# Kernel optimization log

Hardware: AMD Instinct MI355X
Metric: run time of the kernel (lower is better)

## Reference

```python
import jax, jax.numpy as jnp
import numpy as np

D_MODEL = 1024
N_HEADS = 16
D_HEAD = D_MODEL // N_HEADS
B, T = 4, 2048


def layernorm(x, g, b, eps=1e-5):
    mu = jnp.mean(x, axis=-1, keepdims=True)
    var = jnp.mean((x - mu) ** 2, axis=-1, keepdims=True)
    return (x - mu) * jax.lax.rsqrt(var + eps) * g + b


def setup_inputs() -> dict:
    key = jax.random.key(0)
    ks = jax.random.split(key, 12)
    s_in = 1.0 / np.sqrt(D_MODEL)
    s_ff = 1.0 / np.sqrt(4 * D_MODEL)
    return {
        "x": jax.random.normal(ks[0], (B, T, D_MODEL), jnp.float32),
        "Wq": jax.random.normal(ks[1], (N_HEADS, D_MODEL, D_HEAD), jnp.float32) * s_in,
        "Wk": jax.random.normal(ks[2], (N_HEADS, D_MODEL, D_HEAD), jnp.float32) * s_in,
        "Wv": jax.random.normal(ks[3], (N_HEADS, D_MODEL, D_HEAD), jnp.float32) * s_in,
        "Wproj": jax.random.normal(ks[4], (D_MODEL, D_MODEL), jnp.float32) * s_in,
        "bproj": jnp.zeros((D_MODEL,), jnp.float32),
        "W1": jax.random.normal(ks[5], (D_MODEL, 4 * D_MODEL), jnp.float32) * s_in,
        "b1": jnp.zeros((4 * D_MODEL,), jnp.float32),
        "W2": jax.random.normal(ks[6], (4 * D_MODEL, D_MODEL), jnp.float32) * s_ff,
        "b2": jnp.zeros((D_MODEL,), jnp.float32),
        "g1": jnp.ones((D_MODEL,), jnp.float32),
        "beta1": jnp.zeros((D_MODEL,), jnp.float32),
        "g2": jnp.ones((D_MODEL,), jnp.float32),
        "beta2": jnp.zeros((D_MODEL,), jnp.float32),
    }


def reference(x, Wq, Wk, Wv, Wproj, bproj, W1, b1, W2, b2, g1, beta1, g2, beta2):
    Bb, Tt, C = x.shape
    # x = ln1(x); residual uses the NORMALIZED x (quirk of original module)
    x1 = layernorm(x, g1, beta1)
    # all heads at once: [B,H,T,Dh]
    q = jnp.einsum("btd,hdk->bhtk", x1, Wq)
    k = jnp.einsum("btd,hdk->bhtk", x1, Wk)
    v = jnp.einsum("btd,hdk->bhtk", x1, Wv)
    # NOTE: original scales by 1/sqrt(C) with C = d_model, not d_head
    wei = jnp.einsum("bhtk,bhsk->bhts", q, k) / np.sqrt(C).astype(np.float32)
    causal = jnp.tril(jnp.ones((Tt, Tt), bool))
    wei = jnp.where(causal, wei, -jnp.inf)
    wei = jax.nn.softmax(wei, axis=-1)
    attn = jnp.einsum("bhts,bhsk->bhtk", wei, v)  # [B,H,T,Dh]
    attn = attn.transpose(0, 2, 1, 3).reshape(Bb, Tt, C)  # concat heads
    sa = attn @ Wproj + bproj
    x2 = x1 + sa
    # x = ln2(x); residual again uses the normalized tensor
    x3 = layernorm(x2, g2, beta2)
    h = jax.nn.relu(x3 @ W1 + b1)
    ff = h @ W2 + b2
    return x3 + ff
```

## Files before the change

kernel.cpp:

```cpp
#include <hip/hip_runtime.h>
#include <cstdint>

typedef _Float16 f16;
typedef __attribute__((ext_vector_type(8))) _Float16 f16x8;
typedef __attribute__((ext_vector_type(4))) _Float16 f16x4;
typedef __attribute__((ext_vector_type(2))) _Float16 f16x2;
typedef __attribute__((ext_vector_type(4))) float f32x4;
typedef __attribute__((ext_vector_type(16))) float f32x16;

#define D_MODEL 1024
#define T_SEQ   2048
#define NTOK    8192
#define DFF     4096
#define DHEAD   64

struct alignas(16) H8 { f16 h[8]; };

__device__ __forceinline__ void load_lds16(const void* gp, void* lp) {
  __builtin_amdgcn_global_load_lds(
      (const __attribute__((address_space(1))) unsigned int*)(unsigned long long)(uintptr_t)gp,
      (__attribute__((address_space(3))) unsigned int*)(unsigned int)(uintptr_t)lp,
      16, 0, 0);
}

__device__ __forceinline__ void phase_bar() {
  asm volatile("" ::: "memory");
  __builtin_amdgcn_sched_barrier(0);
  __builtin_amdgcn_s_barrier();
  __builtin_amdgcn_sched_barrier(0);
  asm volatile("" ::: "memory");
}

__device__ __forceinline__ void wait_vm2() {
  asm volatile("s_waitcnt vmcnt(2)" ::: "memory");
  __builtin_amdgcn_sched_barrier(0);
}
__device__ __forceinline__ void wait_vm0() {
  asm volatile("s_waitcnt vmcnt(0)" ::: "memory");
  __builtin_amdgcn_sched_barrier(0);
}

__global__ __launch_bounds__(256) void transpose_all(
    const float* __restrict__ Wq, const float* __restrict__ Wk,
    const float* __restrict__ Wv, const float* __restrict__ Wproj,
    const float* __restrict__ W1, const float* __restrict__ W2,
    f16* __restrict__ Wqkv_t, f16* __restrict__ Wproj_t,
    f16* __restrict__ W1_t, f16* __restrict__ W2_t)
{
  __shared__ float tile[32][33];
  int b = blockIdx.x;
  const float* in; f16* out; int rows, cols, r0, c0;
  if (b < 3072) {
    int j = b >> 10;
    int local = b & 1023;
    int slice = local >> 6;
    int tl = local & 63;
    in  = (j == 0 ? Wq : (j == 1 ? Wk : Wv)) + (size_t)slice * 65536;
    out = Wqkv_t + (size_t)j * 1024 * 1024 + (size_t)slice * 65536;
    rows = 1024; cols = 64;
    r0 = (tl & 31) * 32; c0 = (tl >> 5) * 32;
  } else if (b < 4096) {
    int tl = b - 3072;
    in = Wproj; out = Wproj_t; rows = 1024; cols = 1024;
    r0 = (tl & 31) * 32; c0 = (tl >> 5) * 32;
  } else if (b < 8192) {
    int tl = b - 4096;
    in = W1; out = W1_t; rows = 1024; cols = 4096;
    r0 = (tl & 31) * 32; c0 = (tl >> 5) * 32;
  } else {
    int tl = b - 8192;
    in = W2; out = W2_t; rows = 4096; cols = 1024;
    r0 = (tl & 127) * 32; c0 = (tl >> 7) * 32;
  }
  int tx = threadIdx.x & 31, ty = threadIdx.x >> 5;
  #pragma unroll
  for (int i = 0; i < 4; ++i)
    tile[ty + i*8][tx] = in[(size_t)(r0 + ty + i*8)*cols + c0 + tx];
  __syncthreads();
  #pragma unroll
  for (int i = 0; i < 4; ++i)
    out[(size_t)(c0 + ty + i*8)*rows + r0 + tx] = (f16)tile[tx][ty + i*8];
}

__global__ __launch_bounds__(256) void ln_kernel(
    const float* __restrict__ x, const float* __restrict__ g, const float* __restrict__ b,
    float* __restrict__ outf, f16* __restrict__ outh)
{
  int row = blockIdx.x;
  const float* xr = x + (size_t)row * D_MODEL;
  int tid = threadIdx.x;
  float v[4];
  float s = 0.f;
  #pragma unroll
  for (int i = 0; i < 4; ++i) { v[i] = xr[tid + i*256]; s += v[i]; }
  #pragma unroll
  for (int off = 32; off > 0; off >>= 1) s += __shfl_down(s, off, 64);
  __shared__ float red1[4], red2[4];
  if ((tid & 63) == 0) red1[tid >> 6] = s;
  __syncthreads();
  float mean = (red1[0] + red1[1] + red1[2] + red1[3]) * (1.f / D_MODEL);
  float s2 = 0.f;
  #pragma unroll
  for (int i = 0; i < 4; ++i) { float d = v[i] - mean; s2 += d * d; }
  #pragma unroll
  for (int off = 32; off > 0; off >>= 1) s2 += __shfl_down(s2, off, 64);
  if ((tid & 63) == 0) red2[tid >> 6] = s2;
  __syncthreads();
  float var = (red2[0] + red2[1] + red2[2] + red2[3]) * (1.f / D_MODEL);
  float rstd = rsqrtf(var + 1e-5f);
  #pragma unroll
  for (int i = 0; i < 4; ++i) {
    int c = tid + i*256;
    float y = (v[i] - mean) * rstd * g[c] + b[c];
    outf[(size_t)row*D_MODEL + c] = y;
    outh[(size_t)row*D_MODEL + c] = (f16)y;
  }
}


#define STAGE_H(gbase, h, ldst, k0)                                            \
  { _Pragma("unroll")                                                          \
    for (int j_ = 0; j_ < 2; ++j_) {                                           \
      int c_  = tid + j_*512;                                                  \
      int rr_ = c_ >> 3;                                                       \
      int cg_ = (c_ & 7) ^ (rr_ & 7);                                          \
      load_lds16((gbase) + (size_t)((h)*128 + rr_) * K + (k0) + cg_*8,         \
                 (ldst) + (h)*128*64 + (size_t)(c_ & ~63) * 8);                \
    } }

#define LDS_A(bsel, mp)                                                        \
  { _Pragma("unroll")                                                          \
    for (int i_ = 0; i_ < 2; ++i_)                                             \
      _Pragma("unroll")                                                        \
      for (int ks_ = 0; ks_ < 4; ++ks_)                                        \
        fa[i_][ks_] = *(const f16x8*)(&As[bsel][                               \
            (wm + ((mp)*2 + i_)*32 + rl)*64 + (((ks_*2 + hl) ^ sw)*8)]); }

#define LDS_B(bsel, ni, fb)                                                    \
  { _Pragma("unroll")                                                          \
    for (int ks_ = 0; ks_ < 4; ++ks_)                                          \
      fb[ks_] = *(const f16x8*)(&Bs[bsel][                                     \
          (wn + (ni)*32 + rl)*64 + (((ks_*2 + hl) ^ sw)*8)]); }

#define MFMA8(mp, ni, fb)                                                      \
  { __builtin_amdgcn_s_setprio(1);                                             \
    _Pragma("unroll")                                                          \
    for (int ks_ = 0; ks_ < 4; ++ks_) {                                        \
      acc[(mp)*2+0][ni] = __builtin_amdgcn_mfma_f32_32x32x16_f16(              \
          fa[0][ks_], fb[ks_], acc[(mp)*2+0][ni], 0, 0, 0);                    \
      acc[(mp)*2+1][ni] = __builtin_amdgcn_mfma_f32_32x32x16_f16(              \
          fa[1][ks_], fb[ks_], acc[(mp)*2+1][ni], 0, 0, 0);                    \
    }                                                                          \
    __builtin_amdgcn_s_setprio(0); }

template<int MODE, int BN>
__global__ __launch_bounds__(512, 2) void gemm8(
    const f16* __restrict__ A, const f16* __restrict__ BT, int K,
    const float* __restrict__ bias, const float* __restrict__ resid,
    float* __restrict__ outf, f16* __restrict__ o0, f16* __restrict__ o1, f16* __restrict__ o2)
{
  constexpr int BM  = 256;
  constexpr int NWN = BN / 64;
  constexpr int MI  = (BM / (8 / NWN)) / 32;

  __shared__ __align__(16) f16 As[2][BM * 64];
  __shared__ __align__(16) f16 Bs[2][BN * 64];

  int tid  = threadIdx.x;
  int lane = tid & 63;
  int wave = tid >> 6;
  int rl = lane & 31, hl = lane >> 5;
  int sw = rl & 7;
  int wmi = wave / NWN, wni = wave % NWN;
  int wm = wmi * (MI * 32), wn = wni * 64;

  int gx  = gridDim.x;
  int gy  = gridDim.y;
  int nwg = gx * gy;
  int lin = blockIdx.x + gx * blockIdx.y;
  int sid = (nwg & 7) == 0 ? ((lin & 7) * (nwg >> 3) + (lin >> 3)) : lin;
  int bx  = sid / gy, by = sid % gy;

  size_t row0 = (size_t)bx * BM, col0 = (size_t)by * BN;
  const f16* a_base = A  + row0 * K;
  const f16* b_base = BT + col0 * K;
  int NT = K >> 6;

  f32x16 acc[MI][2];
  #pragma unroll
  for (int i = 0; i < MI; ++i)
    #pragma unroll
    for (int j = 0; j < 2; ++j)
      acc[i][j] = (f32x16)(0.f);

  f16x8 fa[2][4], fb0[4], fb1[4];

  if constexpr (BN == 256) {
    STAGE_H(a_base, 0, &As[0][0], 0);
    STAGE_H(a_base, 1, &As[0][0], 0);
    STAGE_H(b_base, 0, &Bs[0][0], 0);
    STAGE_H(b_base, 1, &Bs[0][0], 0);
    if (NT > 1) { STAGE_H(a_base, 0, &As[1][0], 64); wait_vm2(); }
    else        { wait_vm0(); }
    phase_bar();

    for (int t = 0; t < NT; ++t) {
      int cur = t & 1, nxt = cur ^ 1;
      int k1 = (t + 1) << 6, k2 = (t + 2) << 6;
      bool s1 = (t + 1) < NT, s2 = (t + 2) < NT;
      LDS_A(cur, 0); LDS_B(cur, 0, fb0);
      if (s1) STAGE_H(a_base, 1, &As[nxt][0], k1);
      phase_bar();
      MFMA8(0, 0, fb0);
      phase_bar();
      LDS_B(cur, 1, fb1);
      if (s1) STAGE_H(b_base, 0, &Bs[nxt][0], k1);
      phase_bar();
      MFMA8(0, 1, fb1);
      phase_bar();
      LDS_A(cur, 1);
      if (s1) STAGE_H(b_base, 1, &Bs[nxt][0], k1);
      phase_bar();
      MFMA8(1, 0, fb0);
      phase_bar();
      if (s2) STAGE_H(a_base, 0, &As[cur][0], k2);
      phase_bar();
      MFMA8(1, 1, fb1);
      if (s2) wait_vm2(); else wait_vm0();
      phase_bar();
    }
  } else {
    STAGE_H(a_base, 0, &As[0][0], 0);
    STAGE_H(a_base, 1, &As[0][0], 0);
    STAGE_H(b_base, 0, &Bs[0][0], 0);
    if (NT > 1) { STAGE_H(a_base, 0, &As[1][0], 64); wait_vm2(); }
    else        { wait_vm0(); }
    phase_bar();

    for (int t = 0; t < NT; t += 2) {
      int k1 = (t + 1) << 6, k2 = (t + 2) << 6, k3 = (t + 3) << 6;
      bool s1 = (t + 1) < NT, s2 = (t + 2) < NT, s3 = (t + 3) < NT;
      LDS_A(0, 0); LDS_B(0, 0, fb0);
      if (s1) { STAGE_H(a_base, 1, &As[1][0], k1); STAGE_H(b_base, 0, &Bs[1][0], k1); }
      phase_bar();
      MFMA8(0, 0, fb0);
      phase_bar();
      LDS_B(0, 1, fb1);
      if (s2) STAGE_H(a_base, 0, &As[0][0], k2);
      phase_bar();
      MFMA8(0, 1, fb1);
      if (s2) wait_vm2(); else wait_vm0();
      phase_bar();
      if (!s1) break;
      LDS_A(1, 0); LDS_B(1, 0, fb0);
      if (s2) { STAGE_H(a_base, 1, &As[0][0], k2); STAGE_H(b_base, 0, &Bs[0][0], k2); }
      phase_bar();
      MFMA8(0, 0, fb0);
      phase_bar();
      LDS_B(1, 1, fb1);
      if (s3) STAGE_H(a_base, 0, &As[1][0], k3);
      phase_bar();
      MFMA8(0, 1, fb1);
      if (s3) wait_vm2(); else wait_vm0();
      phase_bar();
    }
  }

  int rb = hl * 4;
  #pragma unroll
  for (int mi = 0; mi < MI; ++mi) {
    #pragma unroll
    for (int ni = 0; ni < 2; ++ni) {
      #pragma unroll
      for (int r = 0; r < 16; ++r) {
        size_t grow = row0 + wm + mi*32 + rb + (r & 3) + 8 * (r >> 2);
        size_t gcol = col0 + wn + ni*32 + rl;
        float v = acc[mi][ni][r];
        if constexpr (MODE == 0) {
          int sel = (int)(gcol >> 10);
          int hh  = ((int)gcol >> 6) & 15;
          int dd  = (int)gcol & 63;
          f16* dst = (sel == 0) ? o0 : ((sel == 1) ? o1 : o2);
          if (sel == 0) v *= 0.045084229f;
          size_t bh = (grow >> 11) * 16 + hh;
          dst[(bh * T_SEQ + (grow & 2047)) * DHEAD + dd] = (f16)v;
        } else if constexpr (MODE == 1 || MODE == 3) {
          size_t idx = grow * D_MODEL + gcol;
          outf[idx] = v + bias[gcol] + resid[idx];
        } else {
          float t = v + bias[gcol];
          o0[grow * (size_t)DFF + gcol] = (f16)(t > 0.f ? t : 0.f);
        }
      }
    }
  }
}

__global__ __launch_bounds__(256) void attn_mfma(
    const f16* __restrict__ qb, const f16* __restrict__ kb,
    const f16* __restrict__ vb, f16* __restrict__ attnb)
{
  constexpr int KT  = 64;
  constexpr int LDK = 72;
  __shared__ __align__(16) f16 Kl[2][KT * LDK];
  __shared__ __align__(16) f16 Vt[2][(DHEAD+16) * LDK];
  __shared__ __align__(16) f16 Pt[4 * 32 * LDK];

  int tid  = threadIdx.x;
  int lane = tid & 63, wave = tid >> 6;
  int n    = lane & 15, quad = lane >> 4;
  int quad4 = quad * 4;
  int bh   = blockIdx.x;
  int bxq  = blockIdx.y;

  const f16* qg = qb + (size_t)bh * T_SEQ * DHEAD;
  const f16* kg = kb + (size_t)bh * T_SEQ * DHEAD;
  const f16* vg = vb + (size_t)bh * T_SEQ * DHEAD;
  f16* Ptw = Pt + wave * 32 * LDK;
  size_t orow = (size_t)(bh >> 4) * T_SEQ;
  int hcol = (bh & 15) * DHEAD;

  int skey0 = tid >> 3,  sdq = tid & 7;
  int kp = tid & 31, dblk = tid >> 5;

  {
    int row = 64 + (tid >> 4);
    int colg = (tid & 15) * 4;
    f16 oneval = (f16)((tid >> 4) == 0 ? 1.0f : 0.0f);
    f16x4 fill = {oneval, oneval, oneval, oneval};
    *(f16x4*)(&Vt[0][0] + row * LDK + colg) = fill;
    *(f16x4*)(&Vt[1][0] + row * LDK + colg) = fill;
  }

  #pragma unroll
  for (int pass = 0; pass < 2; ++pass) {
    int qi = pass == 0 ? (15 - bxq) : bxq;
    int qw = qi * 128 + wave * 32;

    f16x8 qfrag[2][2];
    #pragma unroll
    for (int ni = 0; ni < 2; ++ni)
      #pragma unroll
      for (int kj = 0; kj < 2; ++kj)
        qfrag[ni][kj] = *(const f16x8*)(qg + (size_t)(qw + ni*16 + n)*DHEAD + kj*32 + quad*8);

    f32x4 o[2][4];
    f32x4 o4[2];
    #pragma unroll
    for (int mb = 0; mb < 2; ++mb) {
      #pragma unroll
      for (int di = 0; di < 4; ++di) o[mb][di] = f32x4{0.f,0.f,0.f,0.f};
      o4[mb] = f32x4{0.f,0.f,0.f,0.f};
    }

    int ntiles = 2 * qi + 2;

    uint4 kpre0 = *(const uint4*)(kg + (size_t)skey0 * DHEAD + sdq * 8);
    uint4 kpre1 = *(const uint4*)(kg + (size_t)(skey0 + 32) * DHEAD + sdq * 8);
    H8 vpa = *(const H8*)(vg + (size_t)(2*kp) * DHEAD + dblk * 8);
    H8 vpb = *(const H8*)(vg + (size_t)(2*kp) * DHEAD + DHEAD + dblk * 8);
    *(uint4*)(&Kl[0][0] + skey0 * LDK + sdq * 8) = kpre0;
    *(uint4*)(&Kl[0][0] + (skey0 + 32) * LDK + sdq * 8) = kpre1;
    #pragma unroll
    for (int e = 0; e < 8; ++e) {
      f16x2 pk2; pk2[0] = vpa.h[e]; pk2[1] = vpb.h[e];
      *(f16x2*)(&Vt[0][0] + (dblk*8 + e) * LDK + 2*kp) = pk2;
    }
    if (ntiles > 1) {
      kpre0 = *(const uint4*)(kg + (size_t)(KT + skey0) * DHEAD + sdq * 8);
      kpre1 = *(const uint4*)(kg + (size_t)(KT + skey0 + 32) * DHEAD + sdq * 8);
      vpa = *(const H8*)(vg + (size_t)(KT + 2*kp) * DHEAD + dblk * 8);
      vpb = *(const H8*)(vg + (size_t)(KT + 2*kp) * DHEAD + DHEAD + dblk * 8);
    }
    __syncthreads();

    for (int kt = 0; kt < ntiles; ++kt) {
      int kt0 = kt * KT;
      if (kt + 1 < ntiles) {
        f16* Kn = &Kl[(kt + 1) & 1][0];
        f16* Vn = &Vt[(kt + 1) & 1][0];
        *(uint4*)(Kn + skey0 * LDK + sdq * 8) = kpre0;
        *(uint4*)(Kn + (skey0 + 32) * LDK + sdq * 8) = kpre1;
        #pragma unroll
        for (int e = 0; e < 8; ++e) {
          f16x2 pk2; pk2[0] = vpa.h[e]; pk2[1] = vpb.h[e];
          *(f16x2*)(Vn + (dblk*8 + e) * LDK + 2*kp) = pk2;
        }
        if (kt + 2 < ntiles) {
          int nt0 = kt0 + 2 * KT;
          kpre0 = *(const uint4*)(kg + (size_t)(nt0 + skey0) * DHEAD + sdq * 8);
          kpre1 = *(const uint4*)(kg + (size_t)(nt0 + skey0 + 32) * DHEAD + sdq * 8);
          vpa = *(const H8*)(vg + (size_t)(nt0 + 2*kp) * DHEAD + dblk * 8);
          vpb = *(const H8*)(vg + (size_t)(nt0 + 2*kp) * DHEAD + DHEAD + dblk * 8);
        }
      }

      if (kt0 <= qw + 31) {
        const f16* Kc = &Kl[kt & 1][0];
        const f16* Vc = &Vt[kt & 1][0];
        bool need_mask = (kt0 + KT - 1) > qw;

        f32x4 st[4][2];
        #pragma unroll
        for (int mi = 0; mi < 4; ++mi)
          #pragma unroll
          for (int ni = 0; ni < 2; ++ni) st[mi][ni] = f32x4{0.f,0.f,0.f,0.f};
        __builtin_amdgcn_s_setprio(1);
        #pragma unroll
        for (int kj = 0; kj < 2; ++kj) {
          #pragma unroll
          for (int mi = 0; mi < 4; ++mi) {
            f16x8 kf = *(const f16x8*)(Kc + (mi*16 + n) * LDK + kj*32 + quad*8);
            #pragma unroll
            for (int ni = 0; ni < 2; ++ni)
              st[mi][ni] = __builtin_amdgcn_mfma_f32_16x16x32_f16(kf, qfrag[ni][kj], st[mi][ni], 0, 0, 0);
          }
        }
        __builtin_amdgcn_s_setprio(0);

        #pragma unroll
        for (int ni = 0; ni < 2; ++ni) {
          #pragma unroll
          for (int mi = 0; mi < 4; ++mi) {
            float pv[4];
            #pragma unroll
            for (int r = 0; r < 4; ++r) {
              float sv = st[mi][ni][r];
              if (need_mask) {
                int key = kt0 + mi*16 + quad4 + r;
                int qq  = qw  + ni*16 + n;
                if (key > qq) sv = -1e30f;
              }
              pv[r] = __builtin_amdgcn_exp2f(sv);
            }
            f16x2 lo = __builtin_bit_cast(f16x2, __builtin_amdgcn_cvt_pkrtz(pv[0], pv[1]));
            f16x2 hi = __builtin_bit_cast(f16x2, __builtin_amdgcn_cvt_pkrtz(pv[2], pv[3]));
            f16x4 pk; pk[0] = lo[0]; pk[1] = lo[1]; pk[2] = hi[0]; pk[3] = hi[1];
            *(f16x4*)(Ptw + (ni*16 + n) * LDK + mi*16 + quad4) = pk;
          }
        }

        __builtin_amdgcn_s_setprio(1);
        #pragma unroll
        for (int kj = 0; kj < 2; ++kj) {
          f16x8 pf[2];
          #pragma unroll
          for (int mb = 0; mb < 2; ++mb)
            pf[mb] = *(const f16x8*)(Ptw + (mb*16 + n) * LDK + kj*32 + quad*8);
          #pragma unroll
          for (int di = 0; di < 4; ++di) {
            f16x8 vf = *(const f16x8*)(Vc + (di*16 + n) * LDK + kj*32 + quad*8);
            #pragma unroll
            for (int mb = 0; mb < 2; ++mb)
              o[mb][di] = __builtin_amdgcn_mfma_f32_16x16x32_f16(pf[mb], vf, o[mb][di], 0, 0, 0);
          }
          f16x8 vfo = *(const f16x8*)(Vc + (64 + n) * LDK + kj*32 + quad*8);
          #pragma unroll
          for (int mb = 0; mb < 2; ++mb)
            o4[mb] = __builtin_amdgcn_mfma_f32_16x16x32_f16(pf[mb], vfo, o4[mb], 0, 0, 0);
        }
        __builtin_amdgcn_s_setprio(0);
      }
      __syncthreads();
    }

    #pragma unroll
    for (int mb = 0; mb < 2; ++mb) {
      #pragma unroll
      for (int r = 0; r < 4; ++r) {
        float lv  = __shfl(o4[mb][r], quad * 16, 64);
        float inv = 1.f / lv;
        int t = qw + mb*16 + quad4 + r;
        #pragma unroll
        for (int di = 0; di < 4; ++di)
          attnb[(orow + t) * D_MODEL + hcol + di*16 + n] = (f16)(o[mb][di][r] * inv);
      }
    }
  }
}

extern "C" void kernel_launch(void* const* d_in, const int* in_sizes, int n_in,
                              void* d_out, int out_size, void* d_ws, size_t ws_size,
                              hipStream_t stream)
{
  const float* x     = (const float*)d_in[0];
  const float* Wq    = (const float*)d_in[1];
  const float* Wk    = (const float*)d_in[2];
  const float* Wv    = (const float*)d_in[3];
  const float* Wproj = (const float*)d_in[4];
  const float* bproj = (const float*)d_in[5];
  const float* W1    = (const float*)d_in[6];
  const float* b1    = (const float*)d_in[7];
  const float* W2    = (const float*)d_in[8];
  const float* b2    = (const float*)d_in[9];
  const float* g1    = (const float*)d_in[10];
  const float* bt1   = (const float*)d_in[11];
  const float* g2    = (const float*)d_in[12];
  const float* bt2   = (const float*)d_in[13];
  float* out = (float*)d_out;
  (void)in_sizes; (void)n_in; (void)out_size; (void)ws_size;

  char* ws = (char*)d_ws;
  const size_t SZ_H16 = (size_t)NTOK * D_MODEL * 2;
  const size_t SZ_F32 = (size_t)NTOK * D_MODEL * 4;
  f16*   qb      = (f16*)(ws + 0);
  f16*   kb      = (f16*)(ws + 1 * SZ_H16);
  f16*   vb      = (f16*)(ws + 2 * SZ_H16);
  f16*   attnb   = (f16*)(ws + 3 * SZ_H16);
  f16*   hbuf    = (f16*)(ws + 0);
  float* x1f     = (float*)(ws + 4 * SZ_H16);
  f16*   x1h     = (f16*)(ws + 4 * SZ_H16 + SZ_F32);
  float* x3f     = (float*)(ws + 5 * SZ_H16 + SZ_F32);
  f16*   x3h     = (f16*)(ws + 5 * SZ_H16 + 2 * SZ_F32);
  char*  wb      = ws + 6 * SZ_H16 + 2 * SZ_F32;
  f16*   Wqkv_t  = (f16*)(wb);
  f16*   Wproj_t = (f16*)(wb + (size_t)3072*1024*2);
  f16*   W1_t    = (f16*)(wb + (size_t)(3072+1024)*1024*2);
  f16*   W2_t    = (f16*)(wb + (size_t)(3072+1024+4096)*1024*2);

  dim3 blk(256), blk5(512);
  transpose_all<<<dim3(12288), blk, 0, stream>>>(Wq, Wk, Wv, Wproj, W1, W2,
                                                 Wqkv_t, Wproj_t, W1_t, W2_t);
  ln_kernel<<<NTOK, blk, 0, stream>>>(x, g1, bt1, x1f, x1h);
  gemm8<0,128><<<dim3(32, 24), blk5, 0, stream>>>(x1h, Wqkv_t, 1024, nullptr, nullptr, nullptr, qb, kb, vb);
  attn_mfma<<<dim3(64, 8), blk, 0, stream>>>(qb, kb, vb, attnb);
  gemm8<1,128><<<dim3(32, 8), blk5, 0, stream>>>(attnb, Wproj_t, 1024, bproj, x1f, x1f, nullptr, nullptr, nullptr);
  ln_kernel<<<NTOK, blk, 0, stream>>>(x1f, g2, bt2, x3f, x3h);
  gemm8<2,256><<<dim3(32, 16), blk5, 0, stream>>>(x3h, W1_t, 1024, b1, nullptr, nullptr, hbuf, nullptr, nullptr);
  gemm8<3,128><<<dim3(32, 8), blk5, 0, stream>>>(hbuf, W2_t, 4096, b2, x3f, out, nullptr, nullptr, nullptr);
}
```

Before: 472.0 us.

## Split-K the FFN2 GEMM with 256-wide tiles and widen the QKV GEMM tile

The second FFN GEMM now uses 256-wide N tiles split over two K halves via blockIdx.z. One half writes fp32 partials and the other writes fp16 partials, and a new reduce kernel sums them with bias and residual. The QKV projection switches from 128- to 256-wide N tiles. The goal is more data reuse per tile while keeping enough workgroups in flight. The cost is an extra pass over memory for the partials, and the fp16 partial loses precision.

```diff
diff --git a/kernel.cpp b/kernel.cpp
--- a/kernel.cpp
+++ b/kernel.cpp
@@ -117,6 +117,24 @@
   }
 }
 
+__global__ __launch_bounds__(256) void ffn2_reduce(
+    const float* __restrict__ P0, const f16* __restrict__ P1,
+    const float* __restrict__ bias, const float* __restrict__ resid,
+    float* __restrict__ out)
+{
+  size_t i = (size_t)blockIdx.x * 1024 + threadIdx.x * 4;
+  float4 p0 = *(const float4*)(P0 + i);
+  f16x4  p1 = *(const f16x4*)(P1 + i);
+  float4 rs = *(const float4*)(resid + i);
+  float4 bv = *(const float4*)(bias + (i & (D_MODEL - 1)));
+  float4 o;
+  o.x = p0.x + (float)p1[0] + bv.x + rs.x;
+  o.y = p0.y + (float)p1[1] + bv.y + rs.y;
+  o.z = p0.z + (float)p1[2] + bv.z + rs.z;
+  o.w = p0.w + (float)p1[3] + bv.w + rs.w;
+  *(float4*)(out + i) = o;
+}
+
 
 #define STAGE_H(gbase, h, ldst, k0)                                            \
   { _Pragma("unroll")                                                          \
@@ -124,7 +142,7 @@
       int c_  = tid + j_*512;                                                  \
       int rr_ = c_ >> 3;                                                       \
       int cg_ = (c_ & 7) ^ (rr_ & 7);                                          \
-      load_lds16((gbase) + (size_t)((h)*128 + rr_) * K + (k0) + cg_*8,         \
+      load_lds16((gbase) + (size_t)((h)*128 + rr_) * KS + (k0) + cg_*8,        \
                  (ldst) + (h)*128*64 + (size_t)(c_ & ~63) * 8);                \
     } }
 
@@ -155,7 +173,7 @@
 
 template<int MODE, int BN>
 __global__ __launch_bounds__(512, 2) void gemm8(
-    const f16* __restrict__ A, const f16* __restrict__ BT, int K,
+    const f16* __restrict__ A, const f16* __restrict__ BT, int K, int KS,
     const float* __restrict__ bias, const float* __restrict__ resid,
     float* __restrict__ outf, f16* __restrict__ o0, f16* __restrict__ o1, f16* __restrict__ o2)
 {
@@ -181,9 +199,10 @@
   int sid = (nwg & 7) == 0 ? ((lin & 7) * (nwg >> 3) + (lin >> 3)) : lin;
   int bx  = sid / gy, by = sid % gy;
 
+  size_t koff = (size_t)blockIdx.z * (size_t)K;
   size_t row0 = (size_t)bx * BM, col0 = (size_t)by * BN;
-  const f16* a_base = A  + row0 * K;
-  const f16* b_base = BT + col0 * K;
+  const f16* a_base = A  + row0 * KS + koff;
+  const f16* b_base = BT + col0 * KS + koff;
   int NT = K >> 6;
 
   f32x16 acc[MI][2];
@@ -287,9 +306,12 @@
         } else if constexpr (MODE == 1 || MODE == 3) {
           size_t idx = grow * D_MODEL + gcol;
           outf[idx] = v + bias[gcol] + resid[idx];
-        } else {
+        } else if constexpr (MODE == 2) {
           float t = v + bias[gcol];
           o0[grow * (size_t)DFF + gcol] = (f16)(t > 0.f ? t : 0.f);
+        } else {
+          if (blockIdx.z == 0) outf[grow * D_MODEL + gcol] = v;
+          else                 o0[grow * D_MODEL + gcol] = (f16)v;
         }
       }
     }
@@ -517,15 +539,18 @@
   f16*   Wproj_t = (f16*)(wb + (size_t)3072*1024*2);
   f16*   W1_t    = (f16*)(wb + (size_t)(3072+1024)*1024*2);
   f16*   W2_t    = (f16*)(wb + (size_t)(3072+1024+4096)*1024*2);
+  float* pbuf0   = x1f;
+  f16*   pbuf1   = x1h;
 
   dim3 blk(256), blk5(512);
   transpose_all<<<dim3(12288), blk, 0, stream>>>(Wq, Wk, Wv, Wproj, W1, W2,
                                                  Wqkv_t, Wproj_t, W1_t, W2_t);
   ln_kernel<<<NTOK, blk, 0, stream>>>(x, g1, bt1, x1f, x1h);
-  gemm8<0,128><<<dim3(32, 24), blk5, 0, stream>>>(x1h, Wqkv_t, 1024, nullptr, nullptr, nullptr, qb, kb, vb);
+  gemm8<0,256><<<dim3(32, 12), blk5, 0, stream>>>(x1h, Wqkv_t, 1024, 1024, nullptr, nullptr, nullptr, qb, kb, vb);
   attn_mfma<<<dim3(64, 8), blk, 0, stream>>>(qb, kb, vb, attnb);
-  gemm8<1,128><<<dim3(32, 8), blk5, 0, stream>>>(attnb, Wproj_t, 1024, bproj, x1f, x1f, nullptr, nullptr, nullptr);
+  gemm8<1,128><<<dim3(32, 8), blk5, 0, stream>>>(attnb, Wproj_t, 1024, 1024, bproj, x1f, x1f, nullptr, nullptr, nullptr);
   ln_kernel<<<NTOK, blk, 0, stream>>>(x1f, g2, bt2, x3f, x3h);
-  gemm8<2,256><<<dim3(32, 16), blk5, 0, stream>>>(x3h, W1_t, 1024, b1, nullptr, nullptr, hbuf, nullptr, nullptr);
-  gemm8<3,128><<<dim3(32, 8), blk5, 0, stream>>>(hbuf, W2_t, 4096, b2, x3f, out, nullptr, nullptr, nullptr);
-}
+  gemm8<2,256><<<dim3(32, 16), blk5, 0, stream>>>(x3h, W1_t, 1024, 1024, b1, nullptr, nullptr, hbuf, nullptr, nullptr);
+  gemm8<4,256><<<dim3(32, 4, 2), blk5, 0, stream>>>(hbuf, W2_t, 2048, 4096, nullptr, nullptr, pbuf0, pbuf1, nullptr, nullptr);
+  ffn2_reduce<<<dim3(8192), blk, 0, stream>>>(pbuf0, pbuf1, b2, x3f, out);
+}
```

Measured after the change: 517.5 us. 9.6% more time.

## Software-pipeline attention QK^T one tile ahead; add split-K stride to GEMM

Applied to the files above, without the earlier changes.

The attention inner loop now computes the QK^T scores for the next key tile right after the barrier, using two alternating score register sets. The exp/PV work of the current tile can then overlap with the next tile's score MFMAs. The GEMM also gains a separate row stride and a blockIdx.z K-offset in preparation for split-K, but every launch still passes K equal to KS with z=1, so that part does not change behavior. The extra live score registers may raise register pressure and lower occupancy.

```diff
diff --git a/kernel.cpp b/kernel.cpp
--- a/kernel.cpp
+++ b/kernel.cpp
@@ -124,7 +124,7 @@
       int c_  = tid + j_*512;                                                  \
       int rr_ = c_ >> 3;                                                       \
       int cg_ = (c_ & 7) ^ (rr_ & 7);                                          \
-      load_lds16((gbase) + (size_t)((h)*128 + rr_) * K + (k0) + cg_*8,         \
+      load_lds16((gbase) + (size_t)((h)*128 + rr_) * KS + (k0) + cg_*8,        \
                  (ldst) + (h)*128*64 + (size_t)(c_ & ~63) * 8);                \
     } }
 
@@ -155,7 +155,7 @@
 
 template<int MODE, int BN>
 __global__ __launch_bounds__(512, 2) void gemm8(
-    const f16* __restrict__ A, const f16* __restrict__ BT, int K,
+    const f16* __restrict__ A, const f16* __restrict__ BT, int K, int KS,
     const float* __restrict__ bias, const float* __restrict__ resid,
     float* __restrict__ outf, f16* __restrict__ o0, f16* __restrict__ o1, f16* __restrict__ o2)
 {
@@ -181,9 +181,10 @@
   int sid = (nwg & 7) == 0 ? ((lin & 7) * (nwg >> 3) + (lin >> 3)) : lin;
   int bx  = sid / gy, by = sid % gy;
 
+  size_t koff = (size_t)blockIdx.z * (size_t)K;
   size_t row0 = (size_t)bx * BM, col0 = (size_t)by * BN;
-  const f16* a_base = A  + row0 * K;
-  const f16* b_base = BT + col0 * K;
+  const f16* a_base = A  + row0 * KS + koff;
+  const f16* b_base = BT + col0 * KS + koff;
   int NT = K >> 6;
 
   f32x16 acc[MI][2];
@@ -332,6 +333,99 @@
     *(f16x4*)(&Vt[1][0] + row * LDK + colg) = fill;
   }
 
+#define QK_CALC(ktx, stX)                                                      \
+  { const f16* Kc_ = &Kl[(ktx) & 1][0];                                        \
+    _Pragma("unroll")                                                          \
+    for (int mi_ = 0; mi_ < 4; ++mi_)                                          \
+      _Pragma("unroll")                                                        \
+      for (int ni_ = 0; ni_ < 2; ++ni_) stX[mi_][ni_] = f32x4{0.f,0.f,0.f,0.f};\
+    __builtin_amdgcn_s_setprio(1);                                             \
+    _Pragma("unroll")                                                          \
+    for (int kj_ = 0; kj_ < 2; ++kj_) {                                        \
+      _Pragma("unroll")                                                        \
+      for (int mi_ = 0; mi_ < 4; ++mi_) {                                      \
+        f16x8 kf_ = *(const f16x8*)(Kc_ + (mi_*16 + n) * LDK + kj_*32 + quad*8);\
+        _Pragma("unroll")                                                      \
+        for (int ni_ = 0; ni_ < 2; ++ni_)                                      \
+          stX[mi_][ni_] = __builtin_amdgcn_mfma_f32_16x16x32_f16(              \
+              kf_, qfrag[ni_][kj_], stX[mi_][ni_], 0, 0, 0);                   \
+      }                                                                        \
+    }                                                                          \
+    __builtin_amdgcn_s_setprio(0); }
+
+#define ATTN_STEP(kt, stC, stN)                                                \
+  { int kt0_ = (kt) * KT;                                                      \
+    if ((kt) + 1 < ntiles) {                                                   \
+      f16* Kn_ = &Kl[((kt) + 1) & 1][0];                                       \
+      f16* Vn_ = &Vt[((kt) + 1) & 1][0];                                       \
+      *(uint4*)(Kn_ + skey0 * LDK + sdq * 8) = kpre0;                          \
+      *(uint4*)(Kn_ + (skey0 + 32) * LDK + sdq * 8) = kpre1;                   \
+      _Pragma("unroll")                                                        \
+      for (int e_ = 0; e_ < 8; ++e_) {                                         \
+        f16x2 pk2_; pk2_[0] = vpa.h[e_]; pk2_[1] = vpb.h[e_];                  \
+        *(f16x2*)(Vn_ + (dblk*8 + e_) * LDK + 2*kp) = pk2_;                    \
+      }                                                                        \
+      if ((kt) + 2 < ntiles) {                                                 \
+        int nt0_ = kt0_ + 2 * KT;                                              \
+        kpre0 = *(const uint4*)(kg + (size_t)(nt0_ + skey0) * DHEAD + sdq * 8);\
+        kpre1 = *(const uint4*)(kg + (size_t)(nt0_ + skey0 + 32) * DHEAD + sdq * 8);\
+        vpa = *(const H8*)(vg + (size_t)(nt0_ + 2*kp) * DHEAD + dblk * 8);     \
+        vpb = *(const H8*)(vg + (size_t)(nt0_ + 2*kp) * DHEAD + DHEAD + dblk * 8);\
+      }                                                                        \
+    }                                                                          \
+    if (kt0_ <= qw + 31) {                                                     \
+      const f16* Vc_ = &Vt[(kt) & 1][0];                                       \
+      bool need_mask_ = (kt0_ + KT - 1) > qw;                                  \
+      _Pragma("unroll")                                                        \
+      for (int ni_ = 0; ni_ < 2; ++ni_) {                                      \
+        _Pragma("unroll")                                                      \
+        for (int mi_ = 0; mi_ < 4; ++mi_) {                                    \
+          float pv_[4];                                                        \
+          _Pragma("unroll")                                                    \
+          for (int r_ = 0; r_ < 4; ++r_) {                                     \
+            float sv_ = stC[mi_][ni_][r_];                                     \
+            if (need_mask_) {                                                  \
+              int key_ = kt0_ + mi_*16 + quad4 + r_;                           \
+              int qq_  = qw  + ni_*16 + n;                                     \
+              if (key_ > qq_) sv_ = -1e30f;                                    \
+            }                                                                  \
+            pv_[r_] = __builtin_amdgcn_exp2f(sv_);                             \
+          }                                                                    \
+          f16x2 lo_ = __builtin_bit_cast(f16x2, __builtin_amdgcn_cvt_pkrtz(pv_[0], pv_[1]));\
+          f16x2 hi_ = __builtin_bit_cast(f16x2, __builtin_amdgcn_cvt_pkrtz(pv_[2], pv_[3]));\
+          f16x4 pk_; pk_[0] = lo_[0]; pk_[1] = lo_[1]; pk_[2] = hi_[0]; pk_[3] = hi_[1];\
+          *(f16x4*)(Ptw + (ni_*16 + n) * LDK + mi_*16 + quad4) = pk_;          \
+        }                                                                      \
+      }                                                                        \
+      __builtin_amdgcn_s_setprio(1);                                           \
+      _Pragma("unroll")                                                        \
+      for (int kj_ = 0; kj_ < 2; ++kj_) {                                      \
+        f16x8 pf_[2];                                                          \
+        _Pragma("unroll")                                                      \
+        for (int mb_ = 0; mb_ < 2; ++mb_)                                      \
+          pf_[mb_] = *(const f16x8*)(Ptw + (mb_*16 + n) * LDK + kj_*32 + quad*8);\
+        _Pragma("unroll")                                                      \
+        for (int di_ = 0; di_ < 4; ++di_) {                                    \
+          f16x8 vf_ = *(const f16x8*)(Vc_ + (di_*16 + n) * LDK + kj_*32 + quad*8);\
+          _Pragma("unroll")                                                    \
+          for (int mb_ = 0; mb_ < 2; ++mb_)                                    \
+            o[mb_][di_] = __builtin_amdgcn_mfma_f32_16x16x32_f16(              \
+                pf_[mb_], vf_, o[mb_][di_], 0, 0, 0);                          \
+        }                                                                      \
+        f16x8 vfo_ = *(const f16x8*)(Vc_ + (64 + n) * LDK + kj_*32 + quad*8);  \
+        _Pragma("unroll")                                                      \
+        for (int mb_ = 0; mb_ < 2; ++mb_)                                      \
+          o4[mb_] = __builtin_amdgcn_mfma_f32_16x16x32_f16(                    \
+              pf_[mb_], vfo_, o4[mb_], 0, 0, 0);                               \
+      }                                                                        \
+      __builtin_amdgcn_s_setprio(0);                                           \
+    }                                                                          \
+    __syncthreads();                                                           \
+    if ((kt) + 1 < ntiles && kt0_ + KT <= qw + 31) {                           \
+      QK_CALC((kt) + 1, stN);                                                  \
+    }                                                                          \
+  }
+
   #pragma unroll
   for (int pass = 0; pass < 2; ++pass) {
     int qi = pass == 0 ? (15 - bxq) : bxq;
@@ -374,94 +468,12 @@
     }
     __syncthreads();
 
-    for (int kt = 0; kt < ntiles; ++kt) {
-      int kt0 = kt * KT;
-      if (kt + 1 < ntiles) {
-        f16* Kn = &Kl[(kt + 1) & 1][0];
-        f16* Vn = &Vt[(kt + 1) & 1][0];
-        *(uint4*)(Kn + skey0 * LDK + sdq * 8) = kpre0;
-        *(uint4*)(Kn + (skey0 + 32) * LDK + sdq * 8) = kpre1;
-        #pragma unroll
-        for (int e = 0; e < 8; ++e) {
-          f16x2 pk2; pk2[0] = vpa.h[e]; pk2[1] = vpb.h[e];
-          *(f16x2*)(Vn + (dblk*8 + e) * LDK + 2*kp) = pk2;
-        }
-        if (kt + 2 < ntiles) {
-          int nt0 = kt0 + 2 * KT;
-          kpre0 = *(const uint4*)(kg + (size_t)(nt0 + skey0) * DHEAD + sdq * 8);
-          kpre1 = *(const uint4*)(kg + (size_t)(nt0 + skey0 + 32) * DHEAD + sdq * 8);
-          vpa = *(const H8*)(vg + (size_t)(nt0 + 2*kp) * DHEAD + dblk * 8);
-          vpb = *(const H8*)(vg + (size_t)(nt0 + 2*kp) * DHEAD + DHEAD + dblk * 8);
-        }
-      }
-
-      if (kt0 <= qw + 31) {
-        const f16* Kc = &Kl[kt & 1][0];
-        const f16* Vc = &Vt[kt & 1][0];
-        bool need_mask = (kt0 + KT - 1) > qw;
-
-        f32x4 st[4][2];
-        #pragma unroll
-        for (int mi = 0; mi < 4; ++mi)
-          #pragma unroll
-          for (int ni = 0; ni < 2; ++ni) st[mi][ni] = f32x4{0.f,0.f,0.f,0.f};
-        __builtin_amdgcn_s_setprio(1);
-        #pragma unroll
-        for (int kj = 0; kj < 2; ++kj) {
-          #pragma unroll
-          for (int mi = 0; mi < 4; ++mi) {
-            f16x8 kf = *(const f16x8*)(Kc + (mi*16 + n) * LDK + kj*32 + quad*8);
-            #pragma unroll
-            for (int ni = 0; ni < 2; ++ni)
-              st[mi][ni] = __builtin_amdgcn_mfma_f32_16x16x32_f16(kf, qfrag[ni][kj], st[mi][ni], 0, 0, 0);
-          }
-        }
-        __builtin_amdgcn_s_setprio(0);
-
-        #pragma unroll
-        for (int ni = 0; ni < 2; ++ni) {
-          #pragma unroll
-          for (int mi = 0; mi < 4; ++mi) {
-            float pv[4];
-            #pragma unroll
-            for (int r = 0; r < 4; ++r) {
-              float sv = st[mi][ni][r];
-              if (need_mask) {
-                int key = kt0 + mi*16 + quad4 + r;
-                int qq  = qw  + ni*16 + n;
-                if (key > qq) sv = -1e30f;
-              }
-              pv[r] = __builtin_amdgcn_exp2f(sv);
-            }
-            f16x2 lo = __builtin_bit_cast(f16x2, __builtin_amdgcn_cvt_pkrtz(pv[0], pv[1]));
-            f16x2 hi = __builtin_bit_cast(f16x2, __builtin_amdgcn_cvt_pkrtz(pv[2], pv[3]));
-            f16x4 pk; pk[0] = lo[0]; pk[1] = lo[1]; pk[2] = hi[0]; pk[3] = hi[1];
-            *(f16x4*)(Ptw + (ni*16 + n) * LDK + mi*16 + quad4) = pk;
-          }
-        }
-
-        __builtin_amdgcn_s_setprio(1);
-        #pragma unroll
-        for (int kj = 0; kj < 2; ++kj) {
-          f16x8 pf[2];
-          #pragma unroll
-          for (int mb = 0; mb < 2; ++mb)
-            pf[mb] = *(const f16x8*)(Ptw + (mb*16 + n) * LDK + kj*32 + quad*8);
-          #pragma unroll
-          for (int di = 0; di < 4; ++di) {
-            f16x8 vf = *(const f16x8*)(Vc + (di*16 + n) * LDK + kj*32 + quad*8);
-            #pragma unroll
-            for (int mb = 0; mb < 2; ++mb)
-              o[mb][di] = __builtin_amdgcn_mfma_f32_16x16x32_f16(pf[mb], vf, o[mb][di], 0, 0, 0);
-          }
-          f16x8 vfo = *(const f16x8*)(Vc + (64 + n) * LDK + kj*32 + quad*8);
-          #pragma unroll
-          for (int mb = 0; mb < 2; ++mb)
-            o4[mb] = __builtin_amdgcn_mfma_f32_16x16x32_f16(pf[mb], vfo, o4[mb], 0, 0, 0);
-        }
-        __builtin_amdgcn_s_setprio(0);
-      }
-      __syncthreads();
+    f32x4 stA[4][2], stB[4][2];
+    QK_CALC(0, stA);
+
+    for (int kt = 0; kt < ntiles; kt += 2) {
+      ATTN_STEP(kt,     stA, stB);
+      ATTN_STEP(kt + 1, stB, stA);
     }
 
     #pragma unroll
@@ -477,6 +489,8 @@
       }
     }
   }
+#undef QK_CALC
+#undef ATTN_STEP
 }
 
 extern "C" void kernel_launch(void* const* d_in, const int* in_sizes, int n_in,
@@ -522,10 +536,10 @@
   transpose_all<<<dim3(12288), blk, 0, stream>>>(Wq, Wk, Wv, Wproj, W1, W2,
                                                  Wqkv_t, Wproj_t, W1_t, W2_t);
   ln_kernel<<<NTOK, blk, 0, stream>>>(x, g1, bt1, x1f, x1h);
-  gemm8<0,128><<<dim3(32, 24), blk5, 0, stream>>>(x1h, Wqkv_t, 1024, nullptr, nullptr, nullptr, qb, kb, vb);
+  gemm8<0,128><<<dim3(32, 24), blk5, 0, stream>>>(x1h, Wqkv_t, 1024, 1024, nullptr, nullptr, nullptr, qb, kb, vb);
   attn_mfma<<<dim3(64, 8), blk, 0, stream>>>(qb, kb, vb, attnb);
-  gemm8<1,128><<<dim3(32, 8), blk5, 0, stream>>>(attnb, Wproj_t, 1024, bproj, x1f, x1f, nullptr, nullptr, nullptr);
+  gemm8<1,128><<<dim3(32, 8), blk5, 0, stream>>>(attnb, Wproj_t, 1024, 1024, bproj, x1f, x1f, nullptr, nullptr, nullptr);
   ln_kernel<<<NTOK, blk, 0, stream>>>(x1f, g2, bt2, x3f, x3h);
-  gemm8<2,256><<<dim3(32, 16), blk5, 0, stream>>>(x3h, W1_t, 1024, b1, nullptr, nullptr, hbuf, nullptr, nullptr);
-  gemm8<3,128><<<dim3(32, 8), blk5, 0, stream>>>(hbuf, W2_t, 4096, b2, x3f, out, nullptr, nullptr, nullptr);
-}
+  gemm8<2,256><<<dim3(32, 16), blk5, 0, stream>>>(x3h, W1_t, 1024, 1024, b1, nullptr, nullptr, hbuf, nullptr, nullptr);
+  gemm8<3,128><<<dim3(32, 8), blk5, 0, stream>>>(hbuf, W2_t, 4096, 4096, b2, x3f, out, nullptr, nullptr, nullptr);
+}
```

Measured after the change: 514.0 us. +8.9%, slower.
